# Kernel tuning notes

Measured on AMD Instinct MI355X. Metric: run time of the kernel, lower is better.

## Reference

```python
import jax, jax.numpy as jnp
import numpy as np

VAR0, VAR1 = 0.1, 0.2
THRESHOLD = 0.35
NEGPOS_RATIO = 7
LOW_GT_THRESH = 0.2  # match() filters GT whose best prior IoU < 0.2


def setup_inputs() -> dict:
    key = jax.random.key(0)
    ks = jax.random.split(key, 8)
    B, P, G = 16, 43008, 128
    loc_data = jax.random.normal(ks[0], (B, P, 4), jnp.float32)
    conf_data = jax.random.normal(ks[1], (B, P, 2), jnp.float32)
    landm_data = jax.random.normal(ks[2], (B, P, 10), jnp.float32)
    # priors in cxcywh form, positive sizes
    pc = jax.random.uniform(ks[3], (P, 2), jnp.float32)
    pwh = jax.random.uniform(ks[4], (P, 2), jnp.float32, minval=0.02, maxval=0.32)
    priors = jnp.concatenate([pc, pwh], axis=1)
    # targets: valid xyxy boxes + 10 landmark coords + label (face=1)
    ctr = jax.random.uniform(ks[5], (B, G, 2), jnp.float32, minval=0.2, maxval=0.8)
    wh = jax.random.uniform(ks[6], (B, G, 2), jnp.float32, minval=0.05, maxval=0.3)
    boxes = jnp.concatenate([ctr - wh / 2, ctr + wh / 2], axis=-1)
    landms = jax.random.uniform(ks[7], (B, G, 10), jnp.float32)
    labels = jnp.ones((B, G, 1), jnp.float32)
    targets = jnp.concatenate([boxes, landms, labels], axis=-1)
    return {"loc_data": loc_data, "conf_data": conf_data, "landm_data": landm_data,
            "priors": priors, "targets": targets}


def point_form(priors):
    return jnp.concatenate([priors[:, :2] - priors[:, 2:] / 2,
                            priors[:, :2] + priors[:, 2:] / 2], axis=1)


def jaccard(a, b):  # a: [G,4] xyxy, b: [P,4] xyxy -> [G,P]
    lt = jnp.maximum(a[:, None, :2], b[None, :, :2])
    rb = jnp.minimum(a[:, None, 2:], b[None, :, 2:])
    wh = jnp.clip(rb - lt, 0.0)
    inter = wh[..., 0] * wh[..., 1]
    area_a = (a[:, 2] - a[:, 0]) * (a[:, 3] - a[:, 1])
    area_b = (b[:, 2] - b[:, 0]) * (b[:, 3] - b[:, 1])
    return inter / (area_a[:, None] + area_b[None, :] - inter)


def encode(matched, priors):  # matched xyxy [P,4], priors cxcywh [P,4]
    g_cxcy = (matched[:, :2] + matched[:, 2:]) / 2 - priors[:, :2]
    g_cxcy = g_cxcy / (VAR0 * priors[:, 2:])
    g_wh = jnp.log((matched[:, 2:] - matched[:, :2]) / priors[:, 2:]) / VAR1
    return jnp.concatenate([g_cxcy, g_wh], axis=1)


def encode_landm(matched, priors):  # matched [P,10], priors [P,4]
    m = matched.reshape(-1, 5, 2)
    g = (m - priors[:, None, :2]) / (VAR0 * priors[:, None, 2:])
    return g.reshape(-1, 10)


def match_one(truths, labels, landms, priors):
    G = truths.shape[0]
    overlaps = jaccard(truths, point_form(priors))  # [G, P]
    best_prior_overlap = overlaps.max(axis=1)       # [G]
    best_prior_idx = overlaps.argmax(axis=1)        # [G]
    valid = best_prior_overlap >= LOW_GT_THRESH
    any_valid = jnp.any(valid)
    best_truth_overlap = overlaps.max(axis=0)       # [P]
    best_truth_idx = overlaps.argmax(axis=0)        # [P]
    # index_fill_(0, best_prior_idx_filter, 2): ensure each valid GT keeps its best prior
    fill_val = jnp.where(valid, 2.0, best_truth_overlap[best_prior_idx])
    best_truth_overlap = best_truth_overlap.at[best_prior_idx].set(fill_val)
    # best_truth_idx[best_prior_idx[j]] = j for all j
    best_truth_idx = best_truth_idx.at[best_prior_idx].set(jnp.arange(G))
    matches = truths[best_truth_idx]                       # [P,4]
    conf = labels[best_truth_idx].astype(jnp.int32)        # [P]
    conf = jnp.where(best_truth_overlap < THRESHOLD, 0, conf)
    conf = jnp.where(any_valid, conf, 0)  # no valid GT -> all background
    loc = encode(matches, priors)
    landm = encode_landm(landms[best_truth_idx], priors)
    return loc, conf, landm


def smooth_l1(x):
    ax = jnp.abs(x)
    return jnp.where(ax < 1.0, 0.5 * ax * ax, ax - 0.5)


def reference(loc_data, conf_data, landm_data, priors, targets):
    truths = targets[..., :4]
    landms = targets[..., 4:14]
    labels = targets[..., 14]
    loc_t, conf_t, landm_t = jax.vmap(
        lambda t, l, lm: match_one(t, l, lm, priors))(truths, labels, landms)

    # landmark loss over positives
    pos1 = conf_t > 0
    N1 = jnp.maximum(pos1.sum().astype(jnp.float32), 1.0)
    loss_landm = jnp.sum(smooth_l1(landm_data - landm_t) * pos1[..., None])

    # localization loss over positives
    pos = conf_t != 0
    num_pos = pos.sum(axis=1, keepdims=True)  # [B,1]
    loss_l = jnp.sum(smooth_l1(loc_data - loc_t) * pos[..., None])

    # hard negative mining on per-prior CE loss
    lse = jax.scipy.special.logsumexp(conf_data, axis=-1)  # [B,P]
    gathered = jnp.take_along_axis(conf_data, conf_t[..., None], axis=-1)[..., 0]
    ce_all = lse - gathered                                # [B,P] per-prior CE
    mine = jnp.where(pos, 0.0, ce_all)
    loss_idx = jnp.argsort(-mine, axis=1)
    idx_rank = jnp.argsort(loss_idx, axis=1)
    num_neg = jnp.clip(NEGPOS_RATIO * num_pos, None, pos.shape[1] - 1)
    neg = idx_rank < num_neg
    sel = pos | neg
    loss_c = jnp.sum(jnp.where(sel, ce_all, 0.0))

    N = jnp.maximum(num_pos.sum().astype(jnp.float32), 1.0)
    return loss_l / N, loss_c / N, loss_landm / N1
```

## Files before the change

kernel.cpp:

```cpp
#include <hip/hip_runtime.h>
#include <stdint.h>


#define GC 8
#define PPT 4
#define PPI 2

__device__ __forceinline__ float sl1(float x) {
  float a = fabsf(x);
  return a < 1.f ? 0.5f * a * a : a - 0.5f;
}

__device__ __forceinline__ double dwave(double v) {
#pragma unroll
  for (int o = 32; o; o >>= 1) v += __shfl_down(v, o);
  return v;
}

__global__ __launch_bounds__(256) void k_match(
    const float* __restrict__ priors, const float* __restrict__ targets,
    float* __restrict__ bto, int* __restrict__ bti,
    unsigned long long* __restrict__ bp, int P, int G, int NIOU, int PT2,
    int NGC, int PC) {
  int tid = threadIdx.x;
  __shared__ float4 sgt[128];
  __shared__ unsigned long long sred[GC * 256];

  if ((int)blockIdx.x < NIOU) {
    int b = blockIdx.x / PT2, tile = blockIdx.x % PT2;
    int base = tile * (256 * PPI);
    for (int g = tid; g < G; g += 256) {
      const float* t = targets + ((size_t)b * G + g) * 15;
      sgt[g] = make_float4(t[0], t[1], t[2], t[3]);
    }
    __syncthreads();

    float px1[PPI], py1[PPI], px2[PPI], py2[PPI], pa[PPI];
    float bi[PPI], bu[PPI];
    int bidx[PPI];
#pragma unroll
    for (int k = 0; k < PPI; ++k) {
      int p = base + tid + k * 256;
      int pl = p < P ? p : P - 1;
      float4 pr = ((const float4*)priors)[pl];
      px1[k] = pr.x - pr.z * 0.5f; py1[k] = pr.y - pr.w * 0.5f;
      px2[k] = pr.x + pr.z * 0.5f; py2[k] = pr.y + pr.w * 0.5f;
      pa[k] = pr.z * pr.w;
      bi[k] = -1.f; bu[k] = 1.f; bidx[k] = 0;
    }

    for (int g = 0; g < G; g += 2) {
      float4 T0 = sgt[g];
      float4 T1 = sgt[g + 1];
      float A0 = (T0.z - T0.x) * (T0.w - T0.y);
      float A1 = (T1.z - T1.x) * (T1.w - T1.y);
#pragma unroll
      for (int k = 0; k < PPI; ++k) {
        {
          float iw = fminf(T0.z, px2[k]) - fmaxf(T0.x, px1[k]);
          float ih = fminf(T0.w, py2[k]) - fmaxf(T0.y, py1[k]);
          iw = fmaxf(iw, 0.f); ih = fmaxf(ih, 0.f);
          float inter = iw * ih;
          float uni = (A0 + pa[k]) - inter;
          if (inter * bu[k] > bi[k] * uni) { bi[k] = inter; bu[k] = uni; bidx[k] = g; }
        }
        {
          float iw = fminf(T1.z, px2[k]) - fmaxf(T1.x, px1[k]);
          float ih = fminf(T1.w, py2[k]) - fmaxf(T1.y, py1[k]);
          iw = fmaxf(iw, 0.f); ih = fmaxf(ih, 0.f);
          float inter = iw * ih;
          float uni = (A1 + pa[k]) - inter;
          if (inter * bu[k] > bi[k] * uni) { bi[k] = inter; bu[k] = uni; bidx[k] = g + 1; }
        }
      }
    }
#pragma unroll
    for (int k = 0; k < PPI; ++k) {
      int p = base + tid + k * 256;
      if (p < P) {
        bto[(size_t)b * P + p] = bi[k] / bu[k];
        bti[(size_t)b * P + p] = bidx[k];
      }
    }
  } else {
    int bc = blockIdx.x - NIOU;
    int pc = bc % PC;
    int gcb = (bc / PC) % NGC;
    int b = bc / (PC * NGC);
    int g0 = gcb * GC;

    if (tid < GC) {
      int g = g0 + tid;
      float4 v = make_float4(0.f, 0.f, 0.f, 0.f);
      if (g < G) {
        const float* t = targets + ((size_t)b * G + g) * 15;
        v = make_float4(t[0], t[1], t[2], t[3]);
      }
      sgt[tid] = v;
    }
    __syncthreads();

    float gx1[GC], gy1[GC], gx2[GC], gy2[GC], ga[GC];
#pragma unroll
    for (int j = 0; j < GC; ++j) {
      float4 T = sgt[j];
      gx1[j] = T.x; gy1[j] = T.y; gx2[j] = T.z; gy2[j] = T.w;
      ga[j] = (T.z - T.x) * (T.w - T.y);
    }

    int chunk = (P + PC - 1) / PC;
    int ps = pc * chunk;
    int pe = ps + chunk; if (pe > P) pe = P;
    int count = pe - ps;

    float bi[GC], bu[GC];
    unsigned bpp[GC];
#pragma unroll
    for (int j = 0; j < GC; ++j) { bi[j] = 0.f; bu[j] = 1.f; bpp[j] = (unsigned)(ps + tid); }

    for (int i = tid; i < count; i += 512) {
      int p0 = ps + i;
      int i1 = i + 256;
      int p1 = (i1 < count) ? ps + i1 : p0;
      float4 q0 = ((const float4*)priors)[p0];
      float4 q1 = ((const float4*)priors)[p1];
      float ax1 = q0.x - q0.z * 0.5f, ay1 = q0.y - q0.w * 0.5f;
      float ax2 = q0.x + q0.z * 0.5f, ay2 = q0.y + q0.w * 0.5f;
      float aa = q0.z * q0.w;
      float bx1 = q1.x - q1.z * 0.5f, by1 = q1.y - q1.w * 0.5f;
      float bx2 = q1.x + q1.z * 0.5f, by2 = q1.y + q1.w * 0.5f;
      float ba = q1.z * q1.w;
#pragma unroll
      for (int j = 0; j < GC; ++j) {
        {
          float iw = fminf(gx2[j], ax2) - fmaxf(gx1[j], ax1);
          float ih = fminf(gy2[j], ay2) - fmaxf(gy1[j], ay1);
          iw = fmaxf(iw, 0.f); ih = fmaxf(ih, 0.f);
          float inter = iw * ih;
          float uni = (ga[j] + aa) - inter;
          if (inter * bu[j] > bi[j] * uni) { bi[j] = inter; bu[j] = uni; bpp[j] = (unsigned)p0; }
        }
        {
          float iw = fminf(gx2[j], bx2) - fmaxf(gx1[j], bx1);
          float ih = fminf(gy2[j], by2) - fmaxf(gy1[j], by1);
          iw = fmaxf(iw, 0.f); ih = fmaxf(ih, 0.f);
          float inter = iw * ih;
          float uni = (ga[j] + ba) - inter;
          if (inter * bu[j] > bi[j] * uni) { bi[j] = inter; bu[j] = uni; bpp[j] = (unsigned)p1; }
        }
      }
    }

#pragma unroll
    for (int j = 0; j < GC; ++j) {
      float iou = bi[j] / bu[j];
      unsigned long long pk =
          ((unsigned long long)__float_as_uint(iou) << 32) | (unsigned)(~bpp[j]);
      sred[j * 256 + tid] = pk;
    }
    __syncthreads();
    {
      int j = tid >> 5, s = tid & 31;
      unsigned long long m = sred[j * 256 + s];
#pragma unroll
      for (int t = 1; t < 8; ++t) {
        unsigned long long v = sred[j * 256 + s + t * 32];
        if (v > m) m = v;
      }
      __syncthreads();
      sred[j * 256 + s] = m;
    }
    __syncthreads();
    if (tid < GC) {
      unsigned long long m = sred[tid * 256];
      for (int s = 1; s < 32; ++s) {
        unsigned long long v = sred[tid * 256 + s];
        if (v > m) m = v;
      }
      int g = g0 + tid;
      if (g < G) atomicMax(&bp[(size_t)b * G + g], m);
    }
  }
}

__global__ void k_scatter(const unsigned long long* __restrict__ bp,
                          float* __restrict__ bto, int* __restrict__ bti,
                          int* __restrict__ anyv, int P, int G) {
  int b = blockIdx.x, g = threadIdx.x;
  __shared__ unsigned spp[128];
  __shared__ int s_any;
  if (g == 0) s_any = 0;
  __syncthreads();
  unsigned long long m = bp[(size_t)b * G + g];
  unsigned pp = ~(unsigned)m;
  float val = __uint_as_float((unsigned)(m >> 32));
  bool ok = (m != 0ULL);
  float oldv = 0.f;
  if (ok) oldv = bto[(size_t)b * P + pp];
  spp[g] = ok ? pp : 0xFFFFFFFFu;
  if (ok && val >= 0.2f) s_any = 1;
  __syncthreads();
  bool win = ok;
  for (int g2 = g + 1; g2 < G; ++g2)
    if (spp[g2] == pp) win = false;
  if (win) {
    bto[(size_t)b * P + pp] = (val >= 0.2f) ? 2.0f : oldv;
    bti[(size_t)b * P + pp] = g;
  }
  __syncthreads();
  if (g == 0) anyv[b] = s_any;
}

__global__ __launch_bounds__(256) void k_main(
    const float* __restrict__ loc, const float* __restrict__ conf,
    const float* __restrict__ lm, const float* __restrict__ priors,
    const float* __restrict__ targets, const float* __restrict__ bto,
    const int* __restrict__ bti, const int* __restrict__ anyv,
    float* __restrict__ mine, unsigned* __restrict__ h1,
    double* __restrict__ pll, double* __restrict__ pllm,
    double* __restrict__ plc, int* __restrict__ pnp, int P, int G, int PT) {
  int b = blockIdx.x / PT, tile = blockIdx.x % PT;
  int tid = threadIdx.x;
  int p = tile * 256 + tid;

  __shared__ float st[128 * 15];
  __shared__ unsigned hist[1024];
  __shared__ double rs[12];
  __shared__ int ri[4];

  for (int i = tid; i < G * 15; i += 256) st[i] = targets[(size_t)b * G * 15 + i];
  for (int i = tid; i < 1024; i += 256) hist[i] = 0;
  __syncthreads();

  double ll = 0, llm = 0, lc = 0;
  int np = 0;
  if (p < P) {
    size_t idx = (size_t)b * P + p;
    int av = anyv[b];
    float ov = bto[idx];
    int ti = bti[idx];
    bool pos = av && (ov >= 0.35f);

    float2 c = ((const float2*)conf)[idx];
    float mx = fmaxf(c.x, c.y);
    float lse = mx + logf(expf(c.x - mx) + expf(c.y - mx));
    float ce = lse - (pos ? c.y : c.x);
    float mv = pos ? 0.f : ce;
    mine[idx] = mv;
    atomicAdd(&hist[__float_as_uint(mv) >> 21], 1u);

    if (pos) {
      np = 1;
      lc = (double)ce;
      float4 pr = ((const float4*)priors)[p];
      const float* t = st + ti * 15;
      float dx = 0.1f * pr.z, dy = 0.1f * pr.w;
      float gx = ((t[0] + t[2]) * 0.5f - pr.x) / dx;
      float gy = ((t[1] + t[3]) * 0.5f - pr.y) / dy;
      float gw = logf((t[2] - t[0]) / pr.z) * 5.0f;
      float gh = logf((t[3] - t[1]) / pr.w) * 5.0f;
      float4 ld = ((const float4*)loc)[idx];
      ll = (double)(sl1(ld.x - gx) + sl1(ld.y - gy) + sl1(ld.z - gw) +
                    sl1(ld.w - gh));
      const float2* lmd = (const float2*)lm + idx * 5;
      float s = 0.f;
#pragma unroll
      for (int j = 0; j < 5; ++j) {
        float2 lv = lmd[j];
        float ex = (t[4 + 2 * j] - pr.x) / dx;
        float ey = (t[5 + 2 * j] - pr.y) / dy;
        s += sl1(lv.x - ex) + sl1(lv.y - ey);
      }
      llm = (double)s;
    }
  }

  ll = dwave(ll);
  llm = dwave(llm);
  lc = dwave(lc);
#pragma unroll
  for (int o = 32; o; o >>= 1) np += __shfl_down(np, o);
  int lane = tid & 63, wid = tid >> 6;
  if (lane == 0) { rs[wid] = ll; rs[4 + wid] = llm; rs[8 + wid] = lc; ri[wid] = np; }
  __syncthreads();
  if (tid == 0) {
    pll[blockIdx.x] = rs[0] + rs[1] + rs[2] + rs[3];
    pllm[blockIdx.x] = rs[4] + rs[5] + rs[6] + rs[7];
    plc[blockIdx.x] = rs[8] + rs[9] + rs[10] + rs[11];
    pnp[blockIdx.x] = ri[0] + ri[1] + ri[2] + ri[3];
  }
  for (int i = tid; i < 1024; i += 256)
    if (hist[i]) atomicAdd(&h1[(size_t)b * 1024 + i], hist[i]);
}

__global__ __launch_bounds__(256) void k_sel1(const unsigned* __restrict__ h1,
                                              const int* __restrict__ pnp,
                                              int* __restrict__ num_pos, int P,
                                              int PT, int* __restrict__ pfx1,
                                              int* __restrict__ k1,
                                              int* __restrict__ tbits) {
  int b = blockIdx.x, tid = threadIdx.x;
  __shared__ int sn[256];
  int n = 0;
  for (int i = tid; i < PT; i += 256) n += pnp[b * PT + i];
  sn[tid] = n;
  __syncthreads();
  for (int off = 128; off; off >>= 1) {
    if (tid < off) sn[tid] += sn[tid + off];
    __syncthreads();
  }
  int npos = sn[0];
  if (tid == 0) num_pos[b] = npos;

  long long k = 7LL * (long long)npos;
  long long cap = P - 1;
  if (k <= 0) {
    if (tid == 0) { pfx1[b] = -1; k1[b] = 0; }
    return;
  }
  if (k >= cap) {
    if (tid == 0) { pfx1[b] = -2; k1[b] = 0; tbits[b] = 0; }
    return;
  }

  const unsigned* h = h1 + (size_t)b * 1024;
  __shared__ unsigned S[256];
  unsigned p0 = h[tid * 4], p1 = h[tid * 4 + 1], p2 = h[tid * 4 + 2],
           p3 = h[tid * 4 + 3];
  S[tid] = p0 + p1 + p2 + p3;
  __syncthreads();
  for (int off = 1; off < 256; off <<= 1) {
    unsigned add = (tid + off < 256) ? S[tid + off] : 0;
    __syncthreads();
    S[tid] += add;
    __syncthreads();
  }
  int cnt = __syncthreads_count((long long)S[tid] >= k);
  if (cnt == 0) {
    if (tid == 0) { pfx1[b] = -1; k1[b] = 0; }
    return;
  }
  int seg = cnt - 1;
  if (tid == seg) {
    long long cum = (seg + 1 < 256) ? (long long)S[seg + 1] : 0;
    unsigned hv[4] = {p0, p1, p2, p3};
    int bin = seg * 4;
    for (int j = 3; j >= 0; --j) {
      if (cum + hv[j] >= k) { bin = seg * 4 + j; break; }
      cum += hv[j];
    }
    pfx1[b] = bin;
    k1[b] = (int)(k - cum);
  }
}

__global__ __launch_bounds__(256) void k_h2(const float* __restrict__ mine,
                                            const int* __restrict__ pfx1,
                                            unsigned* __restrict__ h2, int P,
                                            int PT4) {
  int b = blockIdx.x / PT4;
  int pf = pfx1[b];
  if (pf < 0) return;
  int base = (blockIdx.x % PT4) * (256 * PPT) + threadIdx.x;
  __shared__ unsigned hist[2048];
  for (int i = threadIdx.x; i < 2048; i += 256) hist[i] = 0;
  __syncthreads();
#pragma unroll
  for (int k = 0; k < PPT; ++k) {
    int p = base + k * 256;
    if (p < P) {
      unsigned bits = __float_as_uint(mine[(size_t)b * P + p]);
      if ((int)(bits >> 21) == pf) atomicAdd(&hist[(bits >> 10) & 2047], 1u);
    }
  }
  __syncthreads();
  for (int i = threadIdx.x; i < 2048; i += 256)
    if (hist[i]) atomicAdd(&h2[(size_t)b * 2048 + i], hist[i]);
}

__global__ __launch_bounds__(256) void k_sel2(const unsigned* __restrict__ h2,
                                              const int* __restrict__ pfx1,
                                              const int* __restrict__ k1,
                                              int* __restrict__ pfx21,
                                              int* __restrict__ k2) {
  int b = blockIdx.x, tid = threadIdx.x;
  int pf = pfx1[b];
  if (pf < 0) {
    if (tid == 0) { pfx21[b] = pf; k2[b] = 0; }
    return;
  }
  const unsigned* h = h2 + (size_t)b * 2048;
  __shared__ unsigned S[256];
  unsigned hv[8];
  unsigned s = 0;
#pragma unroll
  for (int j = 0; j < 8; ++j) { hv[j] = h[tid * 8 + j]; s += hv[j]; }
  S[tid] = s;
  __syncthreads();
  for (int off = 1; off < 256; off <<= 1) {
    unsigned add = (tid + off < 256) ? S[tid + off] : 0;
    __syncthreads();
    S[tid] += add;
    __syncthreads();
  }
  long long k = (long long)k1[b];
  int cnt = __syncthreads_count((long long)S[tid] >= k);
  if (cnt == 0) {
    if (tid == 0) { pfx21[b] = -1; k2[b] = 0; }
    return;
  }
  int seg = cnt - 1;
  if (tid == seg) {
    long long cum = (seg + 1 < 256) ? (long long)S[seg + 1] : 0;
    int bin = seg * 8;
    for (int j = 7; j >= 0; --j) {
      if (cum + hv[j] >= k) { bin = seg * 8 + j; break; }
      cum += hv[j];
    }
    pfx21[b] = (pf << 11) | bin;
    k2[b] = (int)(k - cum);
  }
}

__global__ __launch_bounds__(256) void k_h3(const float* __restrict__ mine,
                                            const int* __restrict__ pfx21,
                                            unsigned* __restrict__ h3, int P,
                                            int PT4) {
  int b = blockIdx.x / PT4;
  int pf = pfx21[b];
  if (pf < 0) return;
  int base = (blockIdx.x % PT4) * (256 * PPT) + threadIdx.x;
  __shared__ unsigned hist[1024];
  for (int i = threadIdx.x; i < 1024; i += 256) hist[i] = 0;
  __syncthreads();
#pragma unroll
  for (int k = 0; k < PPT; ++k) {
    int p = base + k * 256;
    if (p < P) {
      unsigned bits = __float_as_uint(mine[(size_t)b * P + p]);
      if ((int)(bits >> 10) == pf) atomicAdd(&hist[bits & 1023], 1u);
    }
  }
  __syncthreads();
  for (int i = threadIdx.x; i < 1024; i += 256)
    if (hist[i]) atomicAdd(&h3[(size_t)b * 1024 + i], hist[i]);
}

__global__ __launch_bounds__(256) void k_sel3(const unsigned* __restrict__ h3,
                                              const int* __restrict__ pfx21,
                                              const int* __restrict__ k2,
                                              int* __restrict__ tbits,
                                              double* __restrict__ tieadd) {
  int b = blockIdx.x, tid = threadIdx.x;
  int pf = pfx21[b];
  if (pf == -2) return;
  if (pf == -1) {
    if (tid == 0) tbits[b] = -1;
    return;
  }
  const unsigned* h = h3 + (size_t)b * 1024;
  __shared__ unsigned S[256];
  unsigned p0 = h[tid * 4], p1 = h[tid * 4 + 1], p2 = h[tid * 4 + 2],
           p3 = h[tid * 4 + 3];
  S[tid] = p0 + p1 + p2 + p3;
  __syncthreads();
  for (int off = 1; off < 256; off <<= 1) {
    unsigned add = (tid + off < 256) ? S[tid + off] : 0;
    __syncthreads();
    S[tid] += add;
    __syncthreads();
  }
  long long k = (long long)k2[b];
  int cnt = __syncthreads_count((long long)S[tid] >= k);
  if (cnt == 0) {
    if (tid == 0) tbits[b] = -1;
    return;
  }
  int seg = cnt - 1;
  if (tid == seg) {
    long long cum = (seg + 1 < 256) ? (long long)S[seg + 1] : 0;
    unsigned hv[4] = {p0, p1, p2, p3};
    int bin = seg * 4;
    for (int j = 3; j >= 0; --j) {
      if (cum + hv[j] >= k) { bin = seg * 4 + j; break; }
      cum += hv[j];
    }
    unsigned tb = ((unsigned)pf << 10) | (unsigned)bin;
    tbits[b] = (int)tb;
    long long nat = k - cum;
    tieadd[b] = (double)nat * (double)__uint_as_float(tb);
  }
}

__global__ __launch_bounds__(256) void k_fsum(const float* __restrict__ mine,
                                              const int* __restrict__ tbits,
                                              double* __restrict__ pfs, int P,
                                              int PT4) {
  int b = blockIdx.x / PT4;
  int base = (blockIdx.x % PT4) * (256 * PPT) + threadIdx.x;
  unsigned tb = (unsigned)tbits[b];
  double v = 0.0;
#pragma unroll
  for (int k = 0; k < PPT; ++k) {
    int p = base + k * 256;
    if (p < P) {
      unsigned bits = __float_as_uint(mine[(size_t)b * P + p]);
      if (bits > tb) v += (double)__uint_as_float(bits);
    }
  }
  v = dwave(v);
  __shared__ double rs[4];
  int lane = threadIdx.x & 63, wid = threadIdx.x >> 6;
  if (lane == 0) rs[wid] = v;
  __syncthreads();
  if (threadIdx.x == 0) pfs[blockIdx.x] = rs[0] + rs[1] + rs[2] + rs[3];
}

__global__ __launch_bounds__(256) void k_fin(
    const double* __restrict__ pll, const double* __restrict__ pllm,
    const double* __restrict__ plc, const double* __restrict__ pfs,
    const double* __restrict__ tieadd, const int* __restrict__ num_pos,
    float* __restrict__ out, int NBm, int NB4, int B) {
  int tid = threadIdx.x;
  double a = 0, c = 0, d = 0, f = 0, t = 0, n = 0;
  for (int i = tid; i < NBm; i += 256) { a += pll[i]; c += pllm[i]; d += plc[i]; }
  for (int i = tid; i < NB4; i += 256) f += pfs[i];
  for (int i = tid; i < B; i += 256) { t += tieadd[i]; n += (double)num_pos[i]; }
  a = dwave(a); c = dwave(c); d = dwave(d); f = dwave(f); t = dwave(t);
  n = dwave(n);
  __shared__ double rs[6 * 4];
  int lane = tid & 63, wid = tid >> 6;
  if (lane == 0) {
    rs[wid] = a; rs[4 + wid] = c; rs[8 + wid] = d;
    rs[12 + wid] = f; rs[16 + wid] = t; rs[20 + wid] = n;
  }
  __syncthreads();
  if (tid == 0) {
    double A = rs[0] + rs[1] + rs[2] + rs[3];
    double C = rs[4] + rs[5] + rs[6] + rs[7];
    double D = rs[8] + rs[9] + rs[10] + rs[11];
    double F = rs[12] + rs[13] + rs[14] + rs[15];
    double T = rs[16] + rs[17] + rs[18] + rs[19];
    double N = rs[20] + rs[21] + rs[22] + rs[23];
    if (N < 1.0) N = 1.0;
    out[0] = (float)(A / N);
    out[1] = (float)((D + F + T) / N);
    out[2] = (float)(C / N);
  }
}

extern "C" void kernel_launch(void* const* d_in, const int* in_sizes, int n_in,
                              void* d_out, int out_size, void* d_ws,
                              size_t ws_size, hipStream_t stream) {
  const float* loc = (const float*)d_in[0];
  const float* conf = (const float*)d_in[1];
  const float* lm = (const float*)d_in[2];
  const float* priors = (const float*)d_in[3];
  const float* targets = (const float*)d_in[4];

  int P = in_sizes[3] / 4;
  int B = in_sizes[0] / (4 * P);
  int G = in_sizes[4] / (15 * B);
  int PT = (P + 255) / 256;
  int PT2 = (P + 256 * PPI - 1) / (256 * PPI);
  int PT4 = (P + 256 * PPT - 1) / (256 * PPT);
  int NBm = B * PT;
  int NB4 = B * PT4;
  int NGC = (G + GC - 1) / GC;
  int PC = 8;
  int NIOU = B * PT2;
  int NBP = B * NGC * PC;

  char* w = (char*)d_ws;
  size_t off = 0;
  unsigned long long* bp = (unsigned long long*)(w + off);
  off += (size_t)B * G * 8;
  double* tieadd = (double*)(w + off);
  off += (size_t)B * 8;
  int* ctrl = (int*)(w + off);
  off += (size_t)(8 * B) * 4;
  int* anyv = ctrl;
  int* num_pos = ctrl + B;
  int* pfx1 = ctrl + 2 * B;
  int* k1 = ctrl + 3 * B;
  int* pfx21 = ctrl + 4 * B;
  int* k2 = ctrl + 5 * B;
  int* tbits = ctrl + 6 * B;
  unsigned* h1 = (unsigned*)(w + off);
  off += (size_t)B * 1024 * 4;
  unsigned* h2 = (unsigned*)(w + off);
  off += (size_t)B * 2048 * 4;
  unsigned* h3 = (unsigned*)(w + off);
  off += (size_t)B * 1024 * 4;
  size_t clear_bytes = off;
  off = (off + 255) & ~(size_t)255;
  float* bto = (float*)(w + off);
  off += (size_t)B * P * 4;
  int* bti = (int*)(w + off);
  off += (size_t)B * P * 4;
  float* mine = (float*)(w + off);
  off += (size_t)B * P * 4;
  double* pll = (double*)(w + off);
  off += (size_t)NBm * 8;
  double* pllm = (double*)(w + off);
  off += (size_t)NBm * 8;
  double* plc = (double*)(w + off);
  off += (size_t)NBm * 8;
  double* pfs = (double*)(w + off);
  off += (size_t)NB4 * 8;
  int* pnp = (int*)(w + off);
  off += (size_t)NBm * 4;

  hipMemsetAsync(d_ws, 0, clear_bytes, stream);

  k_match<<<NIOU + NBP, 256, 0, stream>>>(priors, targets, bto, bti, bp, P, G,
                                          NIOU, PT2, NGC, PC);
  k_scatter<<<B, G, 0, stream>>>(bp, bto, bti, anyv, P, G);
  k_main<<<B * PT, 256, 0, stream>>>(loc, conf, lm, priors, targets, bto, bti,
                                     anyv, mine, h1, pll, pllm, plc, pnp, P, G,
                                     PT);
  k_sel1<<<B, 256, 0, stream>>>(h1, pnp, num_pos, P, PT, pfx1, k1, tbits);
  k_h2<<<B * PT4, 256, 0, stream>>>(mine, pfx1, h2, P, PT4);
  k_sel2<<<B, 256, 0, stream>>>(h2, pfx1, k1, pfx21, k2);
  k_h3<<<B * PT4, 256, 0, stream>>>(mine, pfx21, h3, P, PT4);
  k_sel3<<<B, 256, 0, stream>>>(h3, pfx21, k2, tbits, tieadd);
  k_fsum<<<B * PT4, 256, 0, stream>>>(mine, tbits, pfs, P, PT4);
  k_fin<<<1, 256, 0, stream>>>(pll, pllm, plc, pfs, tieadd, num_pos,
                               (float*)d_out, NBm, NB4, B);
}
```

Before: 197.8 us.

## Merge radix-select passes into one per-batch kernel and simplify IoU compare

Result: faster. 182.4 us (-7.8%).

```diff
diff --git a/kernel.cpp b/kernel.cpp
--- a/kernel.cpp
+++ b/kernel.cpp
@@ -3,8 +3,7 @@
 
 
 #define GC 8
-#define PPT 4
-#define PPI 2
+#define PPI 3
 
 __device__ __forceinline__ float sl1(float x) {
   float a = fabsf(x);
@@ -20,23 +19,26 @@
 __global__ __launch_bounds__(256) void k_match(
     const float* __restrict__ priors, const float* __restrict__ targets,
     float* __restrict__ bto, int* __restrict__ bti,
-    unsigned long long* __restrict__ bp, int P, int G, int NIOU, int PT2,
+    unsigned long long* __restrict__ bp, int P, int G, int NIOU, int PT3,
     int NGC, int PC) {
   int tid = threadIdx.x;
   __shared__ float4 sgt[128];
+  __shared__ float sga[128];
   __shared__ unsigned long long sred[GC * 256];
 
   if ((int)blockIdx.x < NIOU) {
-    int b = blockIdx.x / PT2, tile = blockIdx.x % PT2;
+    int b = blockIdx.x / PT3, tile = blockIdx.x % PT3;
     int base = tile * (256 * PPI);
     for (int g = tid; g < G; g += 256) {
       const float* t = targets + ((size_t)b * G + g) * 15;
-      sgt[g] = make_float4(t[0], t[1], t[2], t[3]);
+      float x1 = t[0], y1 = t[1], x2 = t[2], y2 = t[3];
+      sgt[g] = make_float4(x1, y1, x2, y2);
+      sga[g] = (x2 - x1) * (y2 - y1);
     }
     __syncthreads();
 
     float px1[PPI], py1[PPI], px2[PPI], py2[PPI], pa[PPI];
-    float bi[PPI], bu[PPI];
+    float bi[PPI], sb[PPI];
     int bidx[PPI];
 #pragma unroll
     for (int k = 0; k < PPI; ++k) {
@@ -46,31 +48,29 @@
       px1[k] = pr.x - pr.z * 0.5f; py1[k] = pr.y - pr.w * 0.5f;
       px2[k] = pr.x + pr.z * 0.5f; py2[k] = pr.y + pr.w * 0.5f;
       pa[k] = pr.z * pr.w;
-      bi[k] = -1.f; bu[k] = 1.f; bidx[k] = 0;
+      bi[k] = 0.f; sb[k] = 1.f; bidx[k] = 0;
     }
 
     for (int g = 0; g < G; g += 2) {
       float4 T0 = sgt[g];
       float4 T1 = sgt[g + 1];
-      float A0 = (T0.z - T0.x) * (T0.w - T0.y);
-      float A1 = (T1.z - T1.x) * (T1.w - T1.y);
+      float A0 = sga[g];
+      float A1 = sga[g + 1];
 #pragma unroll
       for (int k = 0; k < PPI; ++k) {
         {
           float iw = fminf(T0.z, px2[k]) - fmaxf(T0.x, px1[k]);
           float ih = fminf(T0.w, py2[k]) - fmaxf(T0.y, py1[k]);
-          iw = fmaxf(iw, 0.f); ih = fmaxf(ih, 0.f);
-          float inter = iw * ih;
-          float uni = (A0 + pa[k]) - inter;
-          if (inter * bu[k] > bi[k] * uni) { bi[k] = inter; bu[k] = uni; bidx[k] = g; }
+          float inter = fmaxf(iw, 0.f) * fmaxf(ih, 0.f);
+          float S = A0 + pa[k];
+          if (inter * sb[k] > bi[k] * S) { bi[k] = inter; sb[k] = S; bidx[k] = g; }
         }
         {
           float iw = fminf(T1.z, px2[k]) - fmaxf(T1.x, px1[k]);
           float ih = fminf(T1.w, py2[k]) - fmaxf(T1.y, py1[k]);
-          iw = fmaxf(iw, 0.f); ih = fmaxf(ih, 0.f);
-          float inter = iw * ih;
-          float uni = (A1 + pa[k]) - inter;
-          if (inter * bu[k] > bi[k] * uni) { bi[k] = inter; bu[k] = uni; bidx[k] = g + 1; }
+          float inter = fmaxf(iw, 0.f) * fmaxf(ih, 0.f);
+          float S = A1 + pa[k];
+          if (inter * sb[k] > bi[k] * S) { bi[k] = inter; sb[k] = S; bidx[k] = g + 1; }
         }
       }
     }
@@ -78,7 +78,7 @@
     for (int k = 0; k < PPI; ++k) {
       int p = base + tid + k * 256;
       if (p < P) {
-        bto[(size_t)b * P + p] = bi[k] / bu[k];
+        bto[(size_t)b * P + p] = bi[k] / (sb[k] - bi[k]);
         bti[(size_t)b * P + p] = bidx[k];
       }
     }
@@ -113,10 +113,10 @@
     int pe = ps + chunk; if (pe > P) pe = P;
     int count = pe - ps;
 
-    float bi[GC], bu[GC];
+    float bi[GC], sb[GC];
     unsigned bpp[GC];
 #pragma unroll
-    for (int j = 0; j < GC; ++j) { bi[j] = 0.f; bu[j] = 1.f; bpp[j] = (unsigned)(ps + tid); }
+    for (int j = 0; j < GC; ++j) { bi[j] = 0.f; sb[j] = 1.f; bpp[j] = (unsigned)(ps + tid); }
 
     for (int i = tid; i < count; i += 512) {
       int p0 = ps + i;
@@ -135,25 +135,23 @@
         {
           float iw = fminf(gx2[j], ax2) - fmaxf(gx1[j], ax1);
           float ih = fminf(gy2[j], ay2) - fmaxf(gy1[j], ay1);
-          iw = fmaxf(iw, 0.f); ih = fmaxf(ih, 0.f);
-          float inter = iw * ih;
-          float uni = (ga[j] + aa) - inter;
-          if (inter * bu[j] > bi[j] * uni) { bi[j] = inter; bu[j] = uni; bpp[j] = (unsigned)p0; }
+          float inter = fmaxf(iw, 0.f) * fmaxf(ih, 0.f);
+          float S = ga[j] + aa;
+          if (inter * sb[j] > bi[j] * S) { bi[j] = inter; sb[j] = S; bpp[j] = (unsigned)p0; }
         }
         {
           float iw = fminf(gx2[j], bx2) - fmaxf(gx1[j], bx1);
           float ih = fminf(gy2[j], by2) - fmaxf(gy1[j], by1);
-          iw = fmaxf(iw, 0.f); ih = fmaxf(ih, 0.f);
-          float inter = iw * ih;
-          float uni = (ga[j] + ba) - inter;
-          if (inter * bu[j] > bi[j] * uni) { bi[j] = inter; bu[j] = uni; bpp[j] = (unsigned)p1; }
+          float inter = fmaxf(iw, 0.f) * fmaxf(ih, 0.f);
+          float S = ga[j] + ba;
+          if (inter * sb[j] > bi[j] * S) { bi[j] = inter; sb[j] = S; bpp[j] = (unsigned)p1; }
         }
       }
     }
 
 #pragma unroll
     for (int j = 0; j < GC; ++j) {
-      float iou = bi[j] / bu[j];
+      float iou = bi[j] / (sb[j] - bi[j]);
       unsigned long long pk =
           ((unsigned long long)__float_as_uint(iou) << 32) | (unsigned)(~bpp[j]);
       sred[j * 256 + tid] = pk;
@@ -218,21 +216,22 @@
     const int* __restrict__ bti, const int* __restrict__ anyv,
     float* __restrict__ mine, unsigned* __restrict__ h1,
     double* __restrict__ pll, double* __restrict__ pllm,
-    double* __restrict__ plc, int* __restrict__ pnp, int P, int G, int PT) {
+    double* __restrict__ plc, double* __restrict__ msum,
+    int* __restrict__ pnp, int P, int G, int PT) {
   int b = blockIdx.x / PT, tile = blockIdx.x % PT;
   int tid = threadIdx.x;
   int p = tile * 256 + tid;
 
   __shared__ float st[128 * 15];
   __shared__ unsigned hist[1024];
-  __shared__ double rs[12];
+  __shared__ double rs[16];
   __shared__ int ri[4];
 
   for (int i = tid; i < G * 15; i += 256) st[i] = targets[(size_t)b * G * 15 + i];
   for (int i = tid; i < 1024; i += 256) hist[i] = 0;
   __syncthreads();
 
-  double ll = 0, llm = 0, lc = 0;
+  double ll = 0, llm = 0, lc = 0, ms = 0;
   int np = 0;
   if (p < P) {
     size_t idx = (size_t)b * P + p;
@@ -247,6 +246,7 @@
     float ce = lse - (pos ? c.y : c.x);
     float mv = pos ? 0.f : ce;
     mine[idx] = mv;
+    ms = (double)mv;
     atomicAdd(&hist[__float_as_uint(mv) >> 21], 1u);
 
     if (pos) {
@@ -278,39 +278,45 @@
   ll = dwave(ll);
   llm = dwave(llm);
   lc = dwave(lc);
+  ms = dwave(ms);
 #pragma unroll
   for (int o = 32; o; o >>= 1) np += __shfl_down(np, o);
   int lane = tid & 63, wid = tid >> 6;
-  if (lane == 0) { rs[wid] = ll; rs[4 + wid] = llm; rs[8 + wid] = lc; ri[wid] = np; }
+  if (lane == 0) {
+    rs[wid] = ll; rs[4 + wid] = llm; rs[8 + wid] = lc; rs[12 + wid] = ms;
+    ri[wid] = np;
+  }
   __syncthreads();
   if (tid == 0) {
     pll[blockIdx.x] = rs[0] + rs[1] + rs[2] + rs[3];
     pllm[blockIdx.x] = rs[4] + rs[5] + rs[6] + rs[7];
     plc[blockIdx.x] = rs[8] + rs[9] + rs[10] + rs[11];
+    msum[blockIdx.x] = rs[12] + rs[13] + rs[14] + rs[15];
     pnp[blockIdx.x] = ri[0] + ri[1] + ri[2] + ri[3];
   }
   for (int i = tid; i < 1024; i += 256)
     if (hist[i]) atomicAdd(&h1[(size_t)b * 1024 + i], hist[i]);
 }
 
-__global__ __launch_bounds__(256) void k_sel1(const unsigned* __restrict__ h1,
-                                              const int* __restrict__ pnp,
-                                              int* __restrict__ num_pos, int P,
-                                              int PT, int* __restrict__ pfx1,
-                                              int* __restrict__ k1,
-                                              int* __restrict__ tbits) {
+__global__ __launch_bounds__(256) void k_sel1(
+    const unsigned* __restrict__ h1, const int* __restrict__ pnp,
+    const double* __restrict__ msum, int* __restrict__ num_pos,
+    double* __restrict__ msum_b, int P, int PT, int* __restrict__ pfx1,
+    int* __restrict__ k1) {
   int b = blockIdx.x, tid = threadIdx.x;
   __shared__ int sn[256];
+  __shared__ double sm[256];
   int n = 0;
-  for (int i = tid; i < PT; i += 256) n += pnp[b * PT + i];
-  sn[tid] = n;
+  double m = 0;
+  for (int i = tid; i < PT; i += 256) { n += pnp[b * PT + i]; m += msum[b * PT + i]; }
+  sn[tid] = n; sm[tid] = m;
   __syncthreads();
   for (int off = 128; off; off >>= 1) {
-    if (tid < off) sn[tid] += sn[tid + off];
+    if (tid < off) { sn[tid] += sn[tid + off]; sm[tid] += sm[tid + off]; }
     __syncthreads();
   }
   int npos = sn[0];
-  if (tid == 0) num_pos[b] = npos;
+  if (tid == 0) { num_pos[b] = npos; msum_b[b] = sm[0]; }
 
   long long k = 7LL * (long long)npos;
   long long cap = P - 1;
@@ -319,7 +325,7 @@
     return;
   }
   if (k >= cap) {
-    if (tid == 0) { pfx1[b] = -2; k1[b] = 0; tbits[b] = 0; }
+    if (tid == 0) { pfx1[b] = -2; k1[b] = 0; }
     return;
   }
 
@@ -354,185 +360,125 @@
   }
 }
 
-__global__ __launch_bounds__(256) void k_h2(const float* __restrict__ mine,
-                                            const int* __restrict__ pfx1,
-                                            unsigned* __restrict__ h2, int P,
-                                            int PT4) {
-  int b = blockIdx.x / PT4;
+__global__ __launch_bounds__(256) void k_select(
+    const float* __restrict__ mine, const int* __restrict__ pfx1,
+    const int* __restrict__ k1, double* __restrict__ pfs_b, int P) {
+  int b = blockIdx.x, tid = threadIdx.x;
   int pf = pfx1[b];
   if (pf < 0) return;
-  int base = (blockIdx.x % PT4) * (256 * PPT) + threadIdx.x;
-  __shared__ unsigned hist[2048];
-  for (int i = threadIdx.x; i < 2048; i += 256) hist[i] = 0;
-  __syncthreads();
-#pragma unroll
-  for (int k = 0; k < PPT; ++k) {
-    int p = base + k * 256;
-    if (p < P) {
-      unsigned bits = __float_as_uint(mine[(size_t)b * P + p]);
-      if ((int)(bits >> 21) == pf) atomicAdd(&hist[(bits >> 10) & 2047], 1u);
-    }
-  }
-  __syncthreads();
-  for (int i = threadIdx.x; i < 2048; i += 256)
-    if (hist[i]) atomicAdd(&h2[(size_t)b * 2048 + i], hist[i]);
-}
-
-__global__ __launch_bounds__(256) void k_sel2(const unsigned* __restrict__ h2,
-                                              const int* __restrict__ pfx1,
-                                              const int* __restrict__ k1,
-                                              int* __restrict__ pfx21,
-                                              int* __restrict__ k2) {
-  int b = blockIdx.x, tid = threadIdx.x;
-  int pf = pfx1[b];
-  if (pf < 0) {
-    if (tid == 0) { pfx21[b] = pf; k2[b] = 0; }
-    return;
-  }
-  const unsigned* h = h2 + (size_t)b * 2048;
+  const float* mrow = mine + (size_t)b * P;
+
+  __shared__ unsigned hs[2048];
   __shared__ unsigned S[256];
-  unsigned hv[8];
-  unsigned s = 0;
-#pragma unroll
-  for (int j = 0; j < 8; ++j) { hv[j] = h[tid * 8 + j]; s += hv[j]; }
-  S[tid] = s;
-  __syncthreads();
-  for (int off = 1; off < 256; off <<= 1) {
-    unsigned add = (tid + off < 256) ? S[tid + off] : 0;
-    __syncthreads();
-    S[tid] += add;
-    __syncthreads();
-  }
-  long long k = (long long)k1[b];
-  int cnt = __syncthreads_count((long long)S[tid] >= k);
-  if (cnt == 0) {
-    if (tid == 0) { pfx21[b] = -1; k2[b] = 0; }
-    return;
-  }
-  int seg = cnt - 1;
-  if (tid == seg) {
-    long long cum = (seg + 1 < 256) ? (long long)S[seg + 1] : 0;
-    int bin = seg * 8;
-    for (int j = 7; j >= 0; --j) {
-      if (cum + hv[j] >= k) { bin = seg * 8 + j; break; }
-      cum += hv[j];
-    }
-    pfx21[b] = (pf << 11) | bin;
-    k2[b] = (int)(k - cum);
-  }
-}
-
-__global__ __launch_bounds__(256) void k_h3(const float* __restrict__ mine,
-                                            const int* __restrict__ pfx21,
-                                            unsigned* __restrict__ h3, int P,
-                                            int PT4) {
-  int b = blockIdx.x / PT4;
-  int pf = pfx21[b];
-  if (pf < 0) return;
-  int base = (blockIdx.x % PT4) * (256 * PPT) + threadIdx.x;
-  __shared__ unsigned hist[1024];
-  for (int i = threadIdx.x; i < 1024; i += 256) hist[i] = 0;
-  __syncthreads();
-#pragma unroll
-  for (int k = 0; k < PPT; ++k) {
-    int p = base + k * 256;
-    if (p < P) {
-      unsigned bits = __float_as_uint(mine[(size_t)b * P + p]);
-      if ((int)(bits >> 10) == pf) atomicAdd(&hist[bits & 1023], 1u);
-    }
-  }
-  __syncthreads();
-  for (int i = threadIdx.x; i < 1024; i += 256)
-    if (hist[i]) atomicAdd(&h3[(size_t)b * 1024 + i], hist[i]);
-}
-
-__global__ __launch_bounds__(256) void k_sel3(const unsigned* __restrict__ h3,
-                                              const int* __restrict__ pfx21,
-                                              const int* __restrict__ k2,
-                                              int* __restrict__ tbits,
-                                              double* __restrict__ tieadd) {
-  int b = blockIdx.x, tid = threadIdx.x;
-  int pf = pfx21[b];
-  if (pf == -2) return;
-  if (pf == -1) {
-    if (tid == 0) tbits[b] = -1;
-    return;
-  }
-  const unsigned* h = h3 + (size_t)b * 1024;
-  __shared__ unsigned S[256];
-  unsigned p0 = h[tid * 4], p1 = h[tid * 4 + 1], p2 = h[tid * 4 + 2],
-           p3 = h[tid * 4 + 3];
-  S[tid] = p0 + p1 + p2 + p3;
-  __syncthreads();
-  for (int off = 1; off < 256; off <<= 1) {
-    unsigned add = (tid + off < 256) ? S[tid + off] : 0;
-    __syncthreads();
-    S[tid] += add;
-    __syncthreads();
-  }
-  long long k = (long long)k2[b];
-  int cnt = __syncthreads_count((long long)S[tid] >= k);
-  if (cnt == 0) {
-    if (tid == 0) tbits[b] = -1;
-    return;
-  }
-  int seg = cnt - 1;
-  if (tid == seg) {
-    long long cum = (seg + 1 < 256) ? (long long)S[seg + 1] : 0;
-    unsigned hv[4] = {p0, p1, p2, p3};
-    int bin = seg * 4;
-    for (int j = 3; j >= 0; --j) {
-      if (cum + hv[j] >= k) { bin = seg * 4 + j; break; }
-      cum += hv[j];
-    }
-    unsigned tb = ((unsigned)pf << 10) | (unsigned)bin;
-    tbits[b] = (int)tb;
-    long long nat = k - cum;
-    tieadd[b] = (double)nat * (double)__uint_as_float(tb);
-  }
-}
-
-__global__ __launch_bounds__(256) void k_fsum(const float* __restrict__ mine,
-                                              const int* __restrict__ tbits,
-                                              double* __restrict__ pfs, int P,
-                                              int PT4) {
-  int b = blockIdx.x / PT4;
-  int base = (blockIdx.x % PT4) * (256 * PPT) + threadIdx.x;
-  unsigned tb = (unsigned)tbits[b];
+  __shared__ int spf21, sk2;
+  __shared__ unsigned stb;
+  __shared__ double stie;
+  __shared__ double rs[4];
+
+  for (int i = tid; i < 2048; i += 256) hs[i] = 0;
+  __syncthreads();
+  for (int i = tid; i < P; i += 256) {
+    unsigned bits = __float_as_uint(mrow[i]);
+    if ((int)(bits >> 21) == pf) atomicAdd(&hs[(bits >> 10) & 2047], 1u);
+  }
+  __syncthreads();
+  {
+    unsigned hv[8];
+    unsigned s = 0;
+#pragma unroll
+    for (int j = 0; j < 8; ++j) { hv[j] = hs[tid * 8 + j]; s += hv[j]; }
+    S[tid] = s;
+    __syncthreads();
+    for (int off = 1; off < 256; off <<= 1) {
+      unsigned add = (tid + off < 256) ? S[tid + off] : 0;
+      __syncthreads();
+      S[tid] += add;
+      __syncthreads();
+    }
+    long long k = (long long)k1[b];
+    int cnt = __syncthreads_count((long long)S[tid] >= k);
+    int seg = cnt - 1;
+    if (tid == seg) {
+      long long cum = (seg + 1 < 256) ? (long long)S[seg + 1] : 0;
+      int bin = seg * 8;
+      for (int j = 7; j >= 0; --j) {
+        if (cum + hv[j] >= k) { bin = seg * 8 + j; break; }
+        cum += hv[j];
+      }
+      spf21 = (pf << 11) | bin;
+      sk2 = (int)(k - cum);
+    }
+  }
+  __syncthreads();
+  int pf21 = spf21;
+
+  for (int i = tid; i < 1024; i += 256) hs[i] = 0;
+  __syncthreads();
+  for (int i = tid; i < P; i += 256) {
+    unsigned bits = __float_as_uint(mrow[i]);
+    if ((int)(bits >> 10) == pf21) atomicAdd(&hs[bits & 1023], 1u);
+  }
+  __syncthreads();
+  {
+    unsigned p0 = hs[tid * 4], p1 = hs[tid * 4 + 1], p2 = hs[tid * 4 + 2],
+             p3 = hs[tid * 4 + 3];
+    S[tid] = p0 + p1 + p2 + p3;
+    __syncthreads();
+    for (int off = 1; off < 256; off <<= 1) {
+      unsigned add = (tid + off < 256) ? S[tid + off] : 0;
+      __syncthreads();
+      S[tid] += add;
+      __syncthreads();
+    }
+    long long k = (long long)sk2;
+    int cnt = __syncthreads_count((long long)S[tid] >= k);
+    int seg = cnt - 1;
+    if (tid == seg) {
+      long long cum = (seg + 1 < 256) ? (long long)S[seg + 1] : 0;
+      unsigned hv[4] = {p0, p1, p2, p3};
+      int bin = seg * 4;
+      for (int j = 3; j >= 0; --j) {
+        if (cum + hv[j] >= k) { bin = seg * 4 + j; break; }
+        cum += hv[j];
+      }
+      unsigned tb = ((unsigned)pf21 << 10) | (unsigned)bin;
+      stb = tb;
+      stie = (double)(k - cum) * (double)__uint_as_float(tb);
+    }
+  }
+  __syncthreads();
+
+  unsigned tb = stb;
   double v = 0.0;
-#pragma unroll
-  for (int k = 0; k < PPT; ++k) {
-    int p = base + k * 256;
-    if (p < P) {
-      unsigned bits = __float_as_uint(mine[(size_t)b * P + p]);
-      if (bits > tb) v += (double)__uint_as_float(bits);
-    }
+  for (int i = tid; i < P; i += 256) {
+    unsigned bits = __float_as_uint(mrow[i]);
+    if (bits > tb) v += (double)__uint_as_float(bits);
   }
   v = dwave(v);
-  __shared__ double rs[4];
-  int lane = threadIdx.x & 63, wid = threadIdx.x >> 6;
+  int lane = tid & 63, wid = tid >> 6;
   if (lane == 0) rs[wid] = v;
   __syncthreads();
-  if (threadIdx.x == 0) pfs[blockIdx.x] = rs[0] + rs[1] + rs[2] + rs[3];
+  if (tid == 0) pfs_b[b] = rs[0] + rs[1] + rs[2] + rs[3] + stie;
 }
 
 __global__ __launch_bounds__(256) void k_fin(
     const double* __restrict__ pll, const double* __restrict__ pllm,
-    const double* __restrict__ plc, const double* __restrict__ pfs,
-    const double* __restrict__ tieadd, const int* __restrict__ num_pos,
-    float* __restrict__ out, int NBm, int NB4, int B) {
+    const double* __restrict__ plc, const double* __restrict__ pfs_b,
+    const double* __restrict__ msum_b, const int* __restrict__ num_pos,
+    const int* __restrict__ pfx1, float* __restrict__ out, int NBm, int B) {
   int tid = threadIdx.x;
-  double a = 0, c = 0, d = 0, f = 0, t = 0, n = 0;
+  double a = 0, c = 0, d = 0, f = 0, n = 0;
   for (int i = tid; i < NBm; i += 256) { a += pll[i]; c += pllm[i]; d += plc[i]; }
-  for (int i = tid; i < NB4; i += 256) f += pfs[i];
-  for (int i = tid; i < B; i += 256) { t += tieadd[i]; n += (double)num_pos[i]; }
-  a = dwave(a); c = dwave(c); d = dwave(d); f = dwave(f); t = dwave(t);
-  n = dwave(n);
-  __shared__ double rs[6 * 4];
+  for (int i = tid; i < B; i += 256) {
+    f += (pfx1[i] == -2) ? msum_b[i] : pfs_b[i];
+    n += (double)num_pos[i];
+  }
+  a = dwave(a); c = dwave(c); d = dwave(d); f = dwave(f); n = dwave(n);
+  __shared__ double rs[5 * 4];
   int lane = tid & 63, wid = tid >> 6;
   if (lane == 0) {
     rs[wid] = a; rs[4 + wid] = c; rs[8 + wid] = d;
-    rs[12 + wid] = f; rs[16 + wid] = t; rs[20 + wid] = n;
+    rs[12 + wid] = f; rs[16 + wid] = n;
   }
   __syncthreads();
   if (tid == 0) {
@@ -540,11 +486,10 @@
     double C = rs[4] + rs[5] + rs[6] + rs[7];
     double D = rs[8] + rs[9] + rs[10] + rs[11];
     double F = rs[12] + rs[13] + rs[14] + rs[15];
-    double T = rs[16] + rs[17] + rs[18] + rs[19];
-    double N = rs[20] + rs[21] + rs[22] + rs[23];
+    double N = rs[16] + rs[17] + rs[18] + rs[19];
     if (N < 1.0) N = 1.0;
     out[0] = (float)(A / N);
-    out[1] = (float)((D + F + T) / N);
+    out[1] = (float)((D + F) / N);
     out[2] = (float)(C / N);
   }
 }
@@ -562,20 +507,18 @@
   int B = in_sizes[0] / (4 * P);
   int G = in_sizes[4] / (15 * B);
   int PT = (P + 255) / 256;
-  int PT2 = (P + 256 * PPI - 1) / (256 * PPI);
-  int PT4 = (P + 256 * PPT - 1) / (256 * PPT);
+  int PT3 = (P + 256 * PPI - 1) / (256 * PPI);
   int NBm = B * PT;
-  int NB4 = B * PT4;
   int NGC = (G + GC - 1) / GC;
   int PC = 8;
-  int NIOU = B * PT2;
+  int NIOU = B * PT3;
   int NBP = B * NGC * PC;
 
   char* w = (char*)d_ws;
   size_t off = 0;
   unsigned long long* bp = (unsigned long long*)(w + off);
   off += (size_t)B * G * 8;
-  double* tieadd = (double*)(w + off);
+  double* pfs_b = (double*)(w + off);
   off += (size_t)B * 8;
   int* ctrl = (int*)(w + off);
   off += (size_t)(8 * B) * 4;
@@ -583,14 +526,7 @@
   int* num_pos = ctrl + B;
   int* pfx1 = ctrl + 2 * B;
   int* k1 = ctrl + 3 * B;
-  int* pfx21 = ctrl + 4 * B;
-  int* k2 = ctrl + 5 * B;
-  int* tbits = ctrl + 6 * B;
   unsigned* h1 = (unsigned*)(w + off);
-  off += (size_t)B * 1024 * 4;
-  unsigned* h2 = (unsigned*)(w + off);
-  off += (size_t)B * 2048 * 4;
-  unsigned* h3 = (unsigned*)(w + off);
   off += (size_t)B * 1024 * 4;
   size_t clear_bytes = off;
   off = (off + 255) & ~(size_t)255;
@@ -606,25 +542,24 @@
   off += (size_t)NBm * 8;
   double* plc = (double*)(w + off);
   off += (size_t)NBm * 8;
-  double* pfs = (double*)(w + off);
-  off += (size_t)NB4 * 8;
+  double* msum = (double*)(w + off);
+  off += (size_t)NBm * 8;
+  double* msum_b = (double*)(w + off);
+  off += (size_t)B * 8;
   int* pnp = (int*)(w + off);
   off += (size_t)NBm * 4;
 
   hipMemsetAsync(d_ws, 0, clear_bytes, stream);
 
   k_match<<<NIOU + NBP, 256, 0, stream>>>(priors, targets, bto, bti, bp, P, G,
-                                          NIOU, PT2, NGC, PC);
+                                          NIOU, PT3, NGC, PC);
   k_scatter<<<B, G, 0, stream>>>(bp, bto, bti, anyv, P, G);
   k_main<<<B * PT, 256, 0, stream>>>(loc, conf, lm, priors, targets, bto, bti,
-                                     anyv, mine, h1, pll, pllm, plc, pnp, P, G,
-                                     PT);
-  k_sel1<<<B, 256, 0, stream>>>(h1, pnp, num_pos, P, PT, pfx1, k1, tbits);
-  k_h2<<<B * PT4, 256, 0, stream>>>(mine, pfx1, h2, P, PT4);
-  k_sel2<<<B, 256, 0, stream>>>(h2, pfx1, k1, pfx21, k2);
-  k_h3<<<B * PT4, 256, 0, stream>>>(mine, pfx21, h3, P, PT4);
-  k_sel3<<<B, 256, 0, stream>>>(h3, pfx21, k2, tbits, tieadd);
-  k_fsum<<<B * PT4, 256, 0, stream>>>(mine, tbits, pfs, P, PT4);
-  k_fin<<<1, 256, 0, stream>>>(pll, pllm, plc, pfs, tieadd, num_pos,
-                               (float*)d_out, NBm, NB4, B);
-}
+                                     anyv, mine, h1, pll, pllm, plc, msum, pnp,
+                                     P, G, PT);
+  k_sel1<<<B, 256, 0, stream>>>(h1, pnp, msum, num_pos, msum_b, P, PT, pfx1,
+                                k1);
+  k_select<<<B, 256, 0, stream>>>(mine, pfx1, k1, pfs_b, P);
+  k_fin<<<1, 256, 0, stream>>>(pll, pllm, plc, pfs_b, msum_b, num_pos, pfx1,
+                               (float*)d_out, NBm, B);
+}
```
